# Kernel tuning notes

Hardware: AMD Instinct MI355X
Metric: run time of the kernel (lower is better)

The kernel has to match this reference:

```python
import jax, jax.numpy as jnp
import numpy as np

INPUT_DIM = 1024
NUM_HEADS = 16
D_K = 1024
HEAD_DIM = D_K // NUM_HEADS


def setup_inputs() -> dict:
    key = jax.random.key(0)
    ks = jax.random.split(key, 9)
    s_in = 1.0 / np.sqrt(INPUT_DIM)
    s_dk = 1.0 / np.sqrt(D_K)
    return {
        "x": jax.random.normal(ks[0], (2, 2048, INPUT_DIM), dtype=jnp.float32),
        "Wq": jax.random.uniform(ks[1], (INPUT_DIM, D_K), minval=-s_in, maxval=s_in, dtype=jnp.float32),
        "bq": jax.random.uniform(ks[2], (D_K,), minval=-s_in, maxval=s_in, dtype=jnp.float32),
        "Wk": jax.random.uniform(ks[3], (INPUT_DIM, D_K), minval=-s_in, maxval=s_in, dtype=jnp.float32),
        "bk": jax.random.uniform(ks[4], (D_K,), minval=-s_in, maxval=s_in, dtype=jnp.float32),
        "Wv": jax.random.uniform(ks[5], (INPUT_DIM, D_K), minval=-s_in, maxval=s_in, dtype=jnp.float32),
        "bv": jax.random.uniform(ks[6], (D_K,), minval=-s_in, maxval=s_in, dtype=jnp.float32),
        "Wo": jax.random.uniform(ks[7], (D_K, INPUT_DIM), minval=-s_dk, maxval=s_dk, dtype=jnp.float32),
        "bo": jax.random.uniform(ks[8], (INPUT_DIM,), minval=-s_dk, maxval=s_dk, dtype=jnp.float32),
    }


def reference(x, Wq, bq, Wk, bk, Wv, bv, Wo, bo):
    B, S, _ = x.shape
    H, D = NUM_HEADS, HEAD_DIM
    # QKV projections -> [B, H, S, D]
    q = (x @ Wq + bq).reshape(B, S, H, D).transpose(0, 2, 1, 3)
    k = (x @ Wk + bk).reshape(B, S, H, D).transpose(0, 2, 1, 3)
    v = (x @ Wv + bv).reshape(B, S, H, D).transpose(0, 2, 1, 3)
    scores = jnp.einsum("bhsd,bhtd->bhst", q, k) / jnp.sqrt(jnp.asarray(D, x.dtype))
    attn = jax.nn.softmax(scores, axis=-1)
    out = jnp.einsum("bhst,bhtd->bhsd", attn, v)  # [B,H,S,D]
    out = out.transpose(0, 2, 1, 3).reshape(B, S, H * D)
    return out @ Wo + bo
```

## Files before the change

kernel.cpp:

```cpp
#include <hip/hip_runtime.h>
#include <stdint.h>

typedef _Float16 f16;
typedef f16 f16x4 __attribute__((ext_vector_type(4)));
typedef f16 f16x8 __attribute__((ext_vector_type(8)));
typedef float f32x4 __attribute__((ext_vector_type(4)));
typedef float f32x16 __attribute__((ext_vector_type(16)));

#define AS1 __attribute__((address_space(1)))
#define AS3 __attribute__((address_space(3)))

__device__ __forceinline__ void gll16(const void* g, void* l) {
  __builtin_amdgcn_global_load_lds((AS1 void*)g, (AS3 void*)l, 16, 0, 0);
}

__device__ __forceinline__ f32x4 mfma16(f16x8 a, f16x8 b, f32x4 c) {
  return __builtin_amdgcn_mfma_f32_16x16x32_f16(a, b, c, 0, 0, 0);
}
__device__ __forceinline__ f32x16 mfma32(f16x8 a, f16x8 b, f32x16 c) {
  return __builtin_amdgcn_mfma_f32_32x32x16_f16(a, b, c, 0, 0, 0);
}

__device__ __forceinline__ uint32_t pk_rtn(float a, float b) {
  union { f16 h[2]; uint32_t u; } c;
  c.h[0] = (f16)a;
  c.h[1] = (f16)b;
  return c.u;
}

__device__ __forceinline__ void pl32(uint32_t& x, uint32_t& y) {
  asm("v_permlane32_swap_b32 %0, %1" : "+v"(x), "+v"(y));
}

__device__ __forceinline__ f16x8 mk_bfrag(float e0, float e1, float e2, float e3,
                                          float e4, float e5, float e6, float e7) {
  uint32_t x0 = pk_rtn(e0, e1), y0 = pk_rtn(e4, e5);
  uint32_t x1 = pk_rtn(e2, e3), y1 = pk_rtn(e6, e7);
  pl32(x0, y0);
  pl32(x1, y1);
  union { uint32_t w[4]; f16x8 v; } u;
  u.w[0] = x0; u.w[1] = x1; u.w[2] = y0; u.w[3] = y1;
  return u.v;
}

__device__ __forceinline__ f32x16 zero16() {
  f32x16 z;
#pragma unroll
  for (int i = 0; i < 16; i++) z[i] = 0.f;
  return z;
}


__global__ __launch_bounds__(256) void pack_x_k(const float* __restrict__ x,
                                                f16* __restrict__ xh, int n) {
  int i = (blockIdx.x * 256 + threadIdx.x) * 8;
  if (i < n) {
    float4 a = *(const float4*)(x + i);
    float4 b = *(const float4*)(x + i + 4);
    f16x8 o;
    o[0] = (f16)a.x; o[1] = (f16)a.y; o[2] = (f16)a.z; o[3] = (f16)a.w;
    o[4] = (f16)b.x; o[5] = (f16)b.y; o[6] = (f16)b.z; o[7] = (f16)b.w;
    *(f16x8*)(xh + i) = o;
  }
}

__global__ __launch_bounds__(256) void pack_w_k(const float* __restrict__ Wq,
                                                const float* __restrict__ Wk,
                                                const float* __restrict__ Wv,
                                                const float* __restrict__ Wo,
                                                f16* __restrict__ Wt) {
  __shared__ f16 t[64][65];
  const float* W = (blockIdx.z == 0) ? Wq : (blockIdx.z == 1) ? Wk
                   : (blockIdx.z == 2) ? Wv : Wo;
  int n0 = blockIdx.x * 64, k0 = blockIdx.y * 64;
  int tid = threadIdx.x;
  int kr = tid >> 4;
  int nc = (tid & 15) * 4;
#pragma unroll
  for (int i = 0; i < 4; i++) {
    int k = k0 + kr + i * 16;
    float4 w = *(const float4*)(W + (size_t)k * 1024 + n0 + nc);
    t[nc + 0][kr + i * 16] = (f16)w.x;
    t[nc + 1][kr + i * 16] = (f16)w.y;
    t[nc + 2][kr + i * 16] = (f16)w.z;
    t[nc + 3][kr + i * 16] = (f16)w.w;
  }
  __syncthreads();
  int nr = tid >> 2;
  int c0 = (tid & 3) * 16;
  alignas(16) f16 tmp[16];
#pragma unroll
  for (int e = 0; e < 16; e++) tmp[e] = t[nr][c0 + e];
  f16* dst = Wt + (size_t)(blockIdx.z * 1024 + n0 + nr) * 1024 + k0 + c0;
  *(f16x8*)(dst) = *(const f16x8*)(tmp);
  *(f16x8*)(dst + 8) = *(const f16x8*)(tmp + 8);
}

__device__ __forceinline__ void gemm_main(const f16* __restrict__ A,
                                          const f16* __restrict__ B,
                                          int m0, int n0,
                                          f16* Al, f16* Bl,
                                          f32x4 acc[4][4]) {
  const int K = 1024;
  int tid = threadIdx.x;
  int lane = tid & 63, wid = tid >> 6;
  int wr = (wid >> 1) * 64, wc = (wid & 1) * 64;
#pragma unroll
  for (int mi = 0; mi < 4; mi++)
#pragma unroll
    for (int nj = 0; nj < 4; nj++) {
      f32x4 z = {0.f, 0.f, 0.f, 0.f};
      acc[mi][nj] = z;
    }
  int srow = lane >> 3;
  int sgr = (lane & 7) ^ srow;
  int lr = lane & 15, lg = lane >> 4;
  for (int kt = 0; kt < 16; ++kt) {
    __syncthreads();
#pragma unroll
    for (int q = 0; q < 4; q++) {
      int chunk = wid * 4 + q;
      int row = chunk * 8 + srow;
      gll16(A + (size_t)(m0 + row) * K + kt * 64 + sgr * 8, Al + chunk * 512);
      gll16(B + (size_t)(n0 + row) * K + kt * 64 + sgr * 8, Bl + chunk * 512);
    }
    __syncthreads();
#pragma unroll
    for (int kk = 0; kk < 2; kk++) {
      f16x8 af[4], bf[4];
#pragma unroll
      for (int mi = 0; mi < 4; mi++) {
        int row = wr + mi * 16 + lr;
        int gr = (kk * 4 + lg) ^ (row & 7);
        af[mi] = *(const f16x8*)(Al + row * 64 + gr * 8);
      }
#pragma unroll
      for (int nj = 0; nj < 4; nj++) {
        int row = wc + nj * 16 + lr;
        int gr = (kk * 4 + lg) ^ (row & 7);
        bf[nj] = *(const f16x8*)(Bl + row * 64 + gr * 8);
      }
#pragma unroll
      for (int mi = 0; mi < 4; mi++)
#pragma unroll
        for (int nj = 0; nj < 4; nj++)
          acc[mi][nj] = mfma16(af[mi], bf[nj], acc[mi][nj]);
    }
  }
}

__global__ __launch_bounds__(256) void gemm_qkv_k(const f16* __restrict__ Xh,
                                                  const f16* __restrict__ Wt,
                                                  const float* __restrict__ bq,
                                                  const float* __restrict__ bk,
                                                  const float* __restrict__ bv,
                                                  f16* __restrict__ Q,
                                                  f16* __restrict__ Kb,
                                                  f16* __restrict__ Vt) {
  __shared__ f16 Al[128 * 64];
  __shared__ f16 Bl[128 * 64];
  f32x4 acc[4][4];
  int m0 = blockIdx.y * 128, n0 = blockIdx.x * 128;
  gemm_main(Xh, Wt, m0, n0, Al, Bl, acc);

  int lane = threadIdx.x & 63, wid = threadIdx.x >> 6;
  int wr = (wid >> 1) * 64, wc = (wid & 1) * 64;
  int lg = lane >> 4, lc = lane & 15;
  int which = n0 >> 10;
  if (which == 2) {
#pragma unroll
    for (int mi = 0; mi < 4; mi++)
#pragma unroll
      for (int nj = 0; nj < 4; nj++) {
        int nh = (n0 + wc + nj * 16 + lc) & 1023;
        int h = nh >> 6, d = nh & 63;
        float bb = bv[nh];
        int mbase = m0 + wr + mi * 16 + lg * 4;
        int b = mbase >> 11, s = mbase & 2047;
        f16x4 vv;
#pragma unroll
        for (int r = 0; r < 4; r++) vv[r] = (f16)(acc[mi][nj][r] + bb);
        *(f16x4*)(Vt + ((size_t)(b * 16 + h) * 64 + d) * 2048 + s) = vv;
      }
  } else {
    const float* bias = (which == 0) ? bq : bk;
    f16* out = (which == 0) ? Q : Kb;
    float scale = (which == 0) ? 0.1803368801111204f : 1.0f;
#pragma unroll
    for (int mi = 0; mi < 4; mi++)
#pragma unroll
      for (int nj = 0; nj < 4; nj++) {
        int nh = (n0 + wc + nj * 16 + lc) & 1023;
        int h = nh >> 6, d = nh & 63;
        float bb = bias[nh];
#pragma unroll
        for (int r = 0; r < 4; r++) {
          int m = m0 + wr + mi * 16 + lg * 4 + r;
          int b = m >> 11, s = m & 2047;
          float v = (acc[mi][nj][r] + bb) * scale;
          out[((size_t)(b * 16 + h) * 2048 + s) * 64 + d] = (f16)v;
        }
      }
  }
}

__global__ __launch_bounds__(256) void gemm_out_k(const f16* __restrict__ Oh,
                                                  const f16* __restrict__ Wt,
                                                  const float* __restrict__ bo,
                                                  float* __restrict__ out) {
  __shared__ f16 Al[128 * 64];
  __shared__ f16 Bl[128 * 64];
  f32x4 acc[4][4];
  int m0 = blockIdx.y * 128, n0 = blockIdx.x * 128;
  gemm_main(Oh, Wt, m0, n0, Al, Bl, acc);

  int lane = threadIdx.x & 63, wid = threadIdx.x >> 6;
  int wr = (wid >> 1) * 64, wc = (wid & 1) * 64;
  int lg = lane >> 4, lc = lane & 15;
#pragma unroll
  for (int mi = 0; mi < 4; mi++)
#pragma unroll
    for (int nj = 0; nj < 4; nj++) {
      int n = n0 + wc + nj * 16 + lc;
      float bb = bo[n];
#pragma unroll
      for (int r = 0; r < 4; r++) {
        int m = m0 + wr + mi * 16 + lg * 4 + r;
        out[(size_t)m * 1024 + n] = acc[mi][nj][r] + bb;
      }
    }
}

__global__ __launch_bounds__(128) void attn_k(const f16* __restrict__ Q,
                                              const f16* __restrict__ K,
                                              const f16* __restrict__ Vt,
                                              f16* __restrict__ Oh) {
  __shared__ alignas(16) f16 Kl[2][64 * 64];
  __shared__ alignas(16) f16 Vl[2][64 * 64];

  int tid = threadIdx.x, lane = tid & 63, wid = tid >> 6;
  int q5 = lane & 31, hi = lane >> 5;
  int b0 = blockIdx.x;
  int qc = (b0 >> 3) & 31;
  int bh = (b0 & 7) + ((b0 >> 8) << 3);
  int q0w = qc * 64 + wid * 32;

  const f16* Qp = Q + (size_t)bh * 2048 * 64;
  const f16* Kp = K + (size_t)bh * 2048 * 64;
  const f16* Vp = Vt + (size_t)bh * 64 * 2048;

  f16x8 qf0, qf1, qf2, qf3;
  {
    const f16* qr = Qp + (size_t)(q0w + q5) * 64 + hi * 8;
    qf0 = *(const f16x8*)(qr);
    qf1 = *(const f16x8*)(qr + 16);
    qf2 = *(const f16x8*)(qr + 32);
    qf3 = *(const f16x8*)(qr + 48);
  }

  f32x16 o0 = zero16(), o1 = zero16();
  float m = -1e30f, lsum = 0.f;

  int srow = lane >> 3;
  int sg8 = ((lane & 7) ^ srow) * 8;

  auto STAGE = [&](int buf, int t0) {
#pragma unroll
    for (int qi = 0; qi < 4; qi++) {
      int chunk = wid * 4 + qi;
      int row = chunk * 8 + srow;
      gll16(Kp + (size_t)(t0 + row) * 64 + sg8, &Kl[buf][chunk * 512]);
      gll16(Vp + (size_t)row * 2048 + t0 + sg8, &Vl[buf][chunk * 512]);
    }
  };

  STAGE(0, 0);

  int r0 = q5, r1 = 32 + q5;
  int sw = q5 & 7;

  for (int t = 0; t < 32; ++t) {
    int cur = t & 1;
    if (t < 31) {
      STAGE(cur ^ 1, (t + 1) * 64);
      asm volatile("s_waitcnt vmcnt(8)" ::: "memory");
    } else {
      asm volatile("s_waitcnt vmcnt(0)" ::: "memory");
    }
    __builtin_amdgcn_s_barrier();

    const f16* kb = Kl[cur];
    const f16* vb = Vl[cur];

    f32x16 s0 = zero16(), s1 = zero16();
    __builtin_amdgcn_s_setprio(1);
#pragma unroll
    for (int ks = 0; ks < 4; ks++) {
      int g = 2 * ks + hi;
      f16x8 k0 = *(const f16x8*)(kb + r0 * 64 + ((g ^ sw) << 3));
      f16x8 k1 = *(const f16x8*)(kb + r1 * 64 + ((g ^ sw) << 3));
      f16x8 qv = (ks == 0) ? qf0 : (ks == 1) ? qf1 : (ks == 2) ? qf2 : qf3;
      s0 = mfma32(k0, qv, s0);
      s1 = mfma32(k1, qv, s1);
    }
    __builtin_amdgcn_s_setprio(0);

    f16x8 vf0[4], vf1[4];
#pragma unroll
    for (int ks = 0; ks < 4; ks++) {
      int g = 2 * ks + hi;
      vf0[ks] = *(const f16x8*)(vb + r0 * 64 + ((g ^ sw) << 3));
      vf1[ks] = *(const f16x8*)(vb + r1 * 64 + ((g ^ sw) << 3));
    }

    float w[16];
#pragma unroll
    for (int i = 0; i < 16; i++) w[i] = fmaxf(s0[i], s1[i]);
#pragma unroll
    for (int st = 8; st > 0; st >>= 1)
#pragma unroll
      for (int i = 0; i < st; i++) w[i] = fmaxf(w[i], w[i + st]);
    float mx = w[0];
    mx = fmaxf(mx, __shfl_xor(mx, 32));

    if (__any(mx > m)) {
      float mn = fmaxf(m, mx);
      float al = __builtin_amdgcn_exp2f(m - mn);
      m = mn;
      lsum *= al;
#pragma unroll
      for (int i = 0; i < 16; i++) { o0[i] *= al; o1[i] *= al; }
    }
    float su0 = 0.f, su1 = 0.f, su2 = 0.f, su3 = 0.f;
#pragma unroll
    for (int i = 0; i < 16; i += 4) {
      s0[i + 0] = __builtin_amdgcn_exp2f(s0[i + 0] - m); su0 += s0[i + 0];
      s0[i + 1] = __builtin_amdgcn_exp2f(s0[i + 1] - m); su1 += s0[i + 1];
      s0[i + 2] = __builtin_amdgcn_exp2f(s0[i + 2] - m); su2 += s0[i + 2];
      s0[i + 3] = __builtin_amdgcn_exp2f(s0[i + 3] - m); su3 += s0[i + 3];
    }
#pragma unroll
    for (int i = 0; i < 16; i += 4) {
      s1[i + 0] = __builtin_amdgcn_exp2f(s1[i + 0] - m); su0 += s1[i + 0];
      s1[i + 1] = __builtin_amdgcn_exp2f(s1[i + 1] - m); su1 += s1[i + 1];
      s1[i + 2] = __builtin_amdgcn_exp2f(s1[i + 2] - m); su2 += s1[i + 2];
      s1[i + 3] = __builtin_amdgcn_exp2f(s1[i + 3] - m); su3 += s1[i + 3];
    }
    float sum = (su0 + su1) + (su2 + su3);
    sum += __shfl_xor(sum, 32);
    lsum += sum;

    f16x8 pb0 = mk_bfrag(s0[0], s0[1], s0[2], s0[3], s0[4], s0[5], s0[6], s0[7]);
    f16x8 pb1 = mk_bfrag(s0[8], s0[9], s0[10], s0[11], s0[12], s0[13], s0[14], s0[15]);
    f16x8 pb2 = mk_bfrag(s1[0], s1[1], s1[2], s1[3], s1[4], s1[5], s1[6], s1[7]);
    f16x8 pb3 = mk_bfrag(s1[8], s1[9], s1[10], s1[11], s1[12], s1[13], s1[14], s1[15]);

    __builtin_amdgcn_s_setprio(1);
#pragma unroll
    for (int ks = 0; ks < 4; ks++) {
      f16x8 pv = (ks == 0) ? pb0 : (ks == 1) ? pb1 : (ks == 2) ? pb2 : pb3;
      o0 = mfma32(vf0[ks], pv, o0);
      o1 = mfma32(vf1[ks], pv, o1);
    }
    __builtin_amdgcn_s_setprio(0);

    asm volatile("" ::: "memory");
    __builtin_amdgcn_s_barrier();
  }

  float inv = 1.f / lsum;
  int b = bh >> 4, h = bh & 15;
  f16* op = Oh + ((size_t)(b * 2048 + q0w + q5)) * 1024 + h * 64;
#pragma unroll
  for (int qd = 0; qd < 4; qd++) {
    f16x4 w0, w1;
#pragma unroll
    for (int j = 0; j < 4; j++) {
      int r = qd * 4 + j;
      w0[j] = (f16)(o0[r] * inv);
      w1[j] = (f16)(o1[r] * inv);
    }
    int d0 = 8 * qd + 4 * hi;
    *(f16x4*)(op + d0) = w0;
    *(f16x4*)(op + 32 + d0) = w1;
  }
}


extern "C" void kernel_launch(void* const* d_in, const int* in_sizes, int n_in,
                              void* d_out, int out_size, void* d_ws, size_t ws_size,
                              hipStream_t stream) {
  const float* x  = (const float*)d_in[0];
  const float* Wq = (const float*)d_in[1];
  const float* bq = (const float*)d_in[2];
  const float* Wk = (const float*)d_in[3];
  const float* bk = (const float*)d_in[4];
  const float* Wv = (const float*)d_in[5];
  const float* bv = (const float*)d_in[6];
  const float* Wo = (const float*)d_in[7];
  const float* bo = (const float*)d_in[8];
  float* out = (float*)d_out;

  char* ws = (char*)d_ws;
  const size_t MB8 = (size_t)8 << 20;
  f16* Xh = (f16*)(ws + 0 * MB8);
  f16* Wt = (f16*)(ws + 1 * MB8);
  f16* Q  = (f16*)(ws + 2 * MB8);
  f16* Kb = (f16*)(ws + 3 * MB8);
  f16* Vt = (f16*)(ws + 4 * MB8);
  f16* Oh = (f16*)(ws + 5 * MB8);

  pack_x_k<<<dim3(2048), dim3(256), 0, stream>>>(x, Xh, 4096 * 1024);
  pack_w_k<<<dim3(16, 16, 4), dim3(256), 0, stream>>>(Wq, Wk, Wv, Wo, Wt);
  gemm_qkv_k<<<dim3(24, 32), dim3(256), 0, stream>>>(Xh, Wt, bq, bk, bv, Q, Kb, Vt);
  attn_k<<<dim3(1024), dim3(128), 0, stream>>>(Q, Kb, Vt, Oh);
  gemm_out_k<<<dim3(8, 32), dim3(256), 0, stream>>>(Oh, Wt + (size_t)3072 * 1024, bo, out);
}
```

Baseline: 149.6 us.

## Software-pipeline attention loop so PV MFMAs of previous tile overlap current softmax

Restructures the flash-attention inner loop into a prologue, steady state and epilogue. The P·V product for tile t-1 runs in iteration t, interleaved with the exp2 softmax work of tile t, and the O rescale is deferred by one step. V fragments for the previous tile are read into registers before the buffer is restaged. The aim is to hide the exponential math behind matrix work. The cost is more live registers (vp arrays, P fragments), an extra barrier per iteration and a full vmcnt(0) wait that reduces prefetch depth.

After: 147.7 us. No clear change (-1.3%).

```diff
diff --git a/kernel.cpp b/kernel.cpp
--- a/kernel.cpp
+++ b/kernel.cpp
@@ -279,19 +279,17 @@
   int r0 = q5, r1 = 32 + q5;
   int sw = q5 & 7;
 
-  for (int t = 0; t < 32; ++t) {
-    int cur = t & 1;
-    if (t < 31) {
-      STAGE(cur ^ 1, (t + 1) * 64);
-      asm volatile("s_waitcnt vmcnt(8)" ::: "memory");
-    } else {
-      asm volatile("s_waitcnt vmcnt(0)" ::: "memory");
-    }
+  f16x8 vp0[4], vp1[4];
+  f16x8 pbp0, pbp1, pbp2, pbp3;
+  float aprev = 1.f;
+  bool grew_prev = false;
+
+  {
+    asm volatile("s_waitcnt vmcnt(0)" ::: "memory");
     __builtin_amdgcn_s_barrier();
-
-    const f16* kb = Kl[cur];
-    const f16* vb = Vl[cur];
-
+    STAGE(1, 64);
+
+    const f16* kb = Kl[0];
     f32x16 s0 = zero16(), s1 = zero16();
     __builtin_amdgcn_s_setprio(1);
 #pragma unroll
@@ -305,14 +303,6 @@
     }
     __builtin_amdgcn_s_setprio(0);
 
-    f16x8 vf0[4], vf1[4];
-#pragma unroll
-    for (int ks = 0; ks < 4; ks++) {
-      int g = 2 * ks + hi;
-      vf0[ks] = *(const f16x8*)(vb + r0 * 64 + ((g ^ sw) << 3));
-      vf1[ks] = *(const f16x8*)(vb + r1 * 64 + ((g ^ sw) << 3));
-    }
-
     float w[16];
 #pragma unroll
     for (int i = 0; i < 16; i++) w[i] = fmaxf(s0[i], s1[i]);
@@ -322,50 +312,136 @@
       for (int i = 0; i < st; i++) w[i] = fmaxf(w[i], w[i + st]);
     float mx = w[0];
     mx = fmaxf(mx, __shfl_xor(mx, 32));
-
-    if (__any(mx > m)) {
+    m = mx;
+
+    float sA = 0.f, sB = 0.f, sC = 0.f, sD = 0.f;
+#pragma unroll
+    for (int i = 0; i < 8; i++) { s0[i] = __builtin_amdgcn_exp2f(s0[i] - m); sA += s0[i]; }
+#pragma unroll
+    for (int i = 8; i < 16; i++) { s0[i] = __builtin_amdgcn_exp2f(s0[i] - m); sB += s0[i]; }
+#pragma unroll
+    for (int i = 0; i < 8; i++) { s1[i] = __builtin_amdgcn_exp2f(s1[i] - m); sC += s1[i]; }
+#pragma unroll
+    for (int i = 8; i < 16; i++) { s1[i] = __builtin_amdgcn_exp2f(s1[i] - m); sD += s1[i]; }
+    float sum = (sA + sB) + (sC + sD);
+    sum += __shfl_xor(sum, 32);
+    lsum = sum;
+
+    pbp0 = mk_bfrag(s0[0], s0[1], s0[2], s0[3], s0[4], s0[5], s0[6], s0[7]);
+    pbp1 = mk_bfrag(s0[8], s0[9], s0[10], s0[11], s0[12], s0[13], s0[14], s0[15]);
+    pbp2 = mk_bfrag(s1[0], s1[1], s1[2], s1[3], s1[4], s1[5], s1[6], s1[7]);
+    pbp3 = mk_bfrag(s1[8], s1[9], s1[10], s1[11], s1[12], s1[13], s1[14], s1[15]);
+    aprev = 1.f;
+    grew_prev = false;
+  }
+
+  for (int t = 1; t < 32; ++t) {
+    int cur = t & 1;
+    asm volatile("s_waitcnt vmcnt(0)" ::: "memory");
+    __builtin_amdgcn_s_barrier();
+
+    {
+      const f16* vb = Vl[cur ^ 1];
+#pragma unroll
+      for (int ks = 0; ks < 4; ks++) {
+        int g = 2 * ks + hi;
+        vp0[ks] = *(const f16x8*)(vb + r0 * 64 + ((g ^ sw) << 3));
+        vp1[ks] = *(const f16x8*)(vb + r1 * 64 + ((g ^ sw) << 3));
+      }
+    }
+    asm volatile("s_waitcnt lgkmcnt(0)" ::: "memory");
+    __builtin_amdgcn_sched_barrier(0);
+    __builtin_amdgcn_s_barrier();
+    if (t < 31) STAGE(cur ^ 1, (t + 1) * 64);
+
+    const f16* kb = Kl[cur];
+    f32x16 s0 = zero16(), s1 = zero16();
+    __builtin_amdgcn_s_setprio(1);
+#pragma unroll
+    for (int ks = 0; ks < 4; ks++) {
+      int g = 2 * ks + hi;
+      f16x8 k0 = *(const f16x8*)(kb + r0 * 64 + ((g ^ sw) << 3));
+      f16x8 k1 = *(const f16x8*)(kb + r1 * 64 + ((g ^ sw) << 3));
+      f16x8 qv = (ks == 0) ? qf0 : (ks == 1) ? qf1 : (ks == 2) ? qf2 : qf3;
+      s0 = mfma32(k0, qv, s0);
+      s1 = mfma32(k1, qv, s1);
+    }
+    __builtin_amdgcn_s_setprio(0);
+
+    if (grew_prev) {
+#pragma unroll
+      for (int i = 0; i < 16; i++) { o0[i] *= aprev; o1[i] *= aprev; }
+    }
+
+    float w[16];
+#pragma unroll
+    for (int i = 0; i < 16; i++) w[i] = fmaxf(s0[i], s1[i]);
+#pragma unroll
+    for (int st = 8; st > 0; st >>= 1)
+#pragma unroll
+      for (int i = 0; i < st; i++) w[i] = fmaxf(w[i], w[i + st]);
+    float mx = w[0];
+    mx = fmaxf(mx, __shfl_xor(mx, 32));
+    bool grew = __any(mx > m);
+    float al = 1.f;
+    if (grew) {
       float mn = fmaxf(m, mx);
-      float al = __builtin_amdgcn_exp2f(m - mn);
+      al = __builtin_amdgcn_exp2f(m - mn);
       m = mn;
-      lsum *= al;
-#pragma unroll
-      for (int i = 0; i < 16; i++) { o0[i] *= al; o1[i] *= al; }
-    }
-    float su0 = 0.f, su1 = 0.f, su2 = 0.f, su3 = 0.f;
-#pragma unroll
-    for (int i = 0; i < 16; i += 4) {
-      s0[i + 0] = __builtin_amdgcn_exp2f(s0[i + 0] - m); su0 += s0[i + 0];
-      s0[i + 1] = __builtin_amdgcn_exp2f(s0[i + 1] - m); su1 += s0[i + 1];
-      s0[i + 2] = __builtin_amdgcn_exp2f(s0[i + 2] - m); su2 += s0[i + 2];
-      s0[i + 3] = __builtin_amdgcn_exp2f(s0[i + 3] - m); su3 += s0[i + 3];
-    }
-#pragma unroll
-    for (int i = 0; i < 16; i += 4) {
-      s1[i + 0] = __builtin_amdgcn_exp2f(s1[i + 0] - m); su0 += s1[i + 0];
-      s1[i + 1] = __builtin_amdgcn_exp2f(s1[i + 1] - m); su1 += s1[i + 1];
-      s1[i + 2] = __builtin_amdgcn_exp2f(s1[i + 2] - m); su2 += s1[i + 2];
-      s1[i + 3] = __builtin_amdgcn_exp2f(s1[i + 3] - m); su3 += s1[i + 3];
-    }
-    float sum = (su0 + su1) + (su2 + su3);
+    }
+
+    float sA = 0.f, sB = 0.f, sC = 0.f, sD = 0.f;
+    __builtin_amdgcn_s_setprio(1);
+    o0 = mfma32(vp0[0], pbp0, o0);
+    o1 = mfma32(vp1[0], pbp0, o1);
+#pragma unroll
+    for (int i = 0; i < 8; i++) { s0[i] = __builtin_amdgcn_exp2f(s0[i] - m); sA += s0[i]; }
+    o0 = mfma32(vp0[1], pbp1, o0);
+    o1 = mfma32(vp1[1], pbp1, o1);
+#pragma unroll
+    for (int i = 8; i < 16; i++) { s0[i] = __builtin_amdgcn_exp2f(s0[i] - m); sB += s0[i]; }
+    o0 = mfma32(vp0[2], pbp2, o0);
+    o1 = mfma32(vp1[2], pbp2, o1);
+#pragma unroll
+    for (int i = 0; i < 8; i++) { s1[i] = __builtin_amdgcn_exp2f(s1[i] - m); sC += s1[i]; }
+    o0 = mfma32(vp0[3], pbp3, o0);
+    o1 = mfma32(vp1[3], pbp3, o1);
+#pragma unroll
+    for (int i = 8; i < 16; i++) { s1[i] = __builtin_amdgcn_exp2f(s1[i] - m); sD += s1[i]; }
+    __builtin_amdgcn_s_setprio(0);
+
+    float sum = (sA + sB) + (sC + sD);
     sum += __shfl_xor(sum, 32);
-    lsum += sum;
-
-    f16x8 pb0 = mk_bfrag(s0[0], s0[1], s0[2], s0[3], s0[4], s0[5], s0[6], s0[7]);
-    f16x8 pb1 = mk_bfrag(s0[8], s0[9], s0[10], s0[11], s0[12], s0[13], s0[14], s0[15]);
-    f16x8 pb2 = mk_bfrag(s1[0], s1[1], s1[2], s1[3], s1[4], s1[5], s1[6], s1[7]);
-    f16x8 pb3 = mk_bfrag(s1[8], s1[9], s1[10], s1[11], s1[12], s1[13], s1[14], s1[15]);
-
+    lsum = lsum * al + sum;
+
+    pbp0 = mk_bfrag(s0[0], s0[1], s0[2], s0[3], s0[4], s0[5], s0[6], s0[7]);
+    pbp1 = mk_bfrag(s0[8], s0[9], s0[10], s0[11], s0[12], s0[13], s0[14], s0[15]);
+    pbp2 = mk_bfrag(s1[0], s1[1], s1[2], s1[3], s1[4], s1[5], s1[6], s1[7]);
+    pbp3 = mk_bfrag(s1[8], s1[9], s1[10], s1[11], s1[12], s1[13], s1[14], s1[15]);
+    aprev = al;
+    grew_prev = grew;
+  }
+
+  {
+    const f16* vb = Vl[1];
+#pragma unroll
+    for (int ks = 0; ks < 4; ks++) {
+      int g = 2 * ks + hi;
+      vp0[ks] = *(const f16x8*)(vb + r0 * 64 + ((g ^ sw) << 3));
+      vp1[ks] = *(const f16x8*)(vb + r1 * 64 + ((g ^ sw) << 3));
+    }
+    if (grew_prev) {
+#pragma unroll
+      for (int i = 0; i < 16; i++) { o0[i] *= aprev; o1[i] *= aprev; }
+    }
     __builtin_amdgcn_s_setprio(1);
 #pragma unroll
     for (int ks = 0; ks < 4; ks++) {
-      f16x8 pv = (ks == 0) ? pb0 : (ks == 1) ? pb1 : (ks == 2) ? pb2 : pb3;
-      o0 = mfma32(vf0[ks], pv, o0);
-      o1 = mfma32(vf1[ks], pv, o1);
+      f16x8 pv = (ks == 0) ? pbp0 : (ks == 1) ? pbp1 : (ks == 2) ? pbp2 : pbp3;
+      o0 = mfma32(vp0[ks], pv, o0);
+      o1 = mfma32(vp1[ks], pv, o1);
     }
     __builtin_amdgcn_s_setprio(0);
-
-    asm volatile("" ::: "memory");
-    __builtin_amdgcn_s_barrier();
   }
 
   float inv = 1.f / lsum;
```

## Split attention KV tiles across two waves per query chunk and merge partial softmax

Applied to the files above, without the earlier changes.

The attention kernel now launches 256 threads per block. Two waves cover each 32-query chunk, and each of the pair handles half of every 64-key tile: 32 keys, one score MFMA chain and half the PV work. At the end the two partial (m, l, O) states are combined through LDS with a log-sum-exp style merge before writing fp16 output. Staging is redistributed so two waves load K and two load V, with a 4-way swizzle for the 32-wide V tile. The aim is more waves in flight and shorter per-wave critical paths, at the cost of an extra LDS reduction, doubled per-wave softmax bookkeeping and more barriers.

Result: faster. 144.0 us (-3.7%).

```diff
diff --git a/kernel.cpp b/kernel.cpp
--- a/kernel.cpp
+++ b/kernel.cpp
@@ -231,93 +231,102 @@
     }
 }
 
-__global__ __launch_bounds__(128) void attn_k(const f16* __restrict__ Q,
-                                              const f16* __restrict__ K,
-                                              const f16* __restrict__ Vt,
-                                              f16* __restrict__ Oh) {
-  __shared__ alignas(16) f16 Kl[2][64 * 64];
-  __shared__ alignas(16) f16 Vl[2][64 * 64];
+__global__ __launch_bounds__(256, 4) void attn_k(const f16* __restrict__ Q,
+                                                 const f16* __restrict__ K,
+                                                 const f16* __restrict__ Vt,
+                                                 f16* __restrict__ Oh) {
+  __shared__ alignas(16) char lds_raw[32768];
+  f16* Kl = (f16*)lds_raw;
+  f16* Vl = (f16*)(lds_raw + 16384);
 
   int tid = threadIdx.x, lane = tid & 63, wid = tid >> 6;
   int q5 = lane & 31, hi = lane >> 5;
+  int qc2 = wid >> 1, hv = wid & 1;
   int b0 = blockIdx.x;
   int qc = (b0 >> 3) & 31;
   int bh = (b0 & 7) + ((b0 >> 8) << 3);
-  int q0w = qc * 64 + wid * 32;
+  int q0w = qc * 64 + qc2 * 32;
 
   const f16* Qp = Q + (size_t)bh * 2048 * 64;
   const f16* Kp = K + (size_t)bh * 2048 * 64;
   const f16* Vp = Vt + (size_t)bh * 64 * 2048;
 
-  f16x8 qf0, qf1, qf2, qf3;
+  f16x8 qf[4];
   {
     const f16* qr = Qp + (size_t)(q0w + q5) * 64 + hi * 8;
-    qf0 = *(const f16x8*)(qr);
-    qf1 = *(const f16x8*)(qr + 16);
-    qf2 = *(const f16x8*)(qr + 32);
-    qf3 = *(const f16x8*)(qr + 48);
+#pragma unroll
+    for (int ks = 0; ks < 4; ks++) qf[ks] = *(const f16x8*)(qr + ks * 16);
   }
 
   f32x16 o0 = zero16(), o1 = zero16();
   float m = -1e30f, lsum = 0.f;
 
-  int srow = lane >> 3;
-  int sg8 = ((lane & 7) ^ srow) * 8;
-
-  auto STAGE = [&](int buf, int t0) {
-#pragma unroll
-    for (int qi = 0; qi < 4; qi++) {
-      int chunk = wid * 4 + qi;
-      int row = chunk * 8 + srow;
-      gll16(Kp + (size_t)(t0 + row) * 64 + sg8, &Kl[buf][chunk * 512]);
-      gll16(Vp + (size_t)row * 2048 + t0 + sg8, &Vl[buf][chunk * 512]);
+  int role = wid;
+  int srole = role & 1;
+  int srow8 = lane >> 3, swz8 = ((lane & 7) ^ srow8) * 8;
+  int srow4 = lane >> 2, swz4 = ((lane & 3) ^ (srow4 & 3)) * 8;
+  const f16* sK = Kp + (size_t)(srole * 1024 + srow8) * 64 + swz8;
+  const f16* sV = Vp + (size_t)srow4 * 2048 + srole * 1024 + swz4;
+
+  auto STAGE = [&](int buf, int t) {
+    if (role < 2) {
+      const f16* s = sK + (size_t)t * 32 * 64;
+      f16* d = Kl + buf * 4096 + srole * 2048;
+#pragma unroll
+      for (int c = 0; c < 4; c++) gll16(s + c * 512, d + c * 512);
+    } else {
+      const f16* s = sV + t * 32;
+      f16* d = Vl + buf * 4096 + srole * 2048;
+#pragma unroll
+      for (int c = 0; c < 4; c++) gll16(s + (size_t)c * 16 * 2048, d + c * 512);
     }
   };
 
+  int kqoff[4];
+#pragma unroll
+  for (int ks = 0; ks < 4; ks++) kqoff[ks] = q5 * 64 + (((2 * ks + hi) ^ (q5 & 7)) << 3);
+  int r0 = q5, r1 = q5 + 32;
+  int voff0[2], voff1[2];
+#pragma unroll
+  for (int ks = 0; ks < 2; ks++) {
+    voff0[ks] = r0 * 32 + (((2 * ks + hi) ^ (r0 & 3)) << 3);
+    voff1[ks] = r1 * 32 + (((2 * ks + hi) ^ (r1 & 3)) << 3);
+  }
+
   STAGE(0, 0);
-
-  int r0 = q5, r1 = 32 + q5;
-  int sw = q5 & 7;
 
   for (int t = 0; t < 32; ++t) {
     int cur = t & 1;
     if (t < 31) {
-      STAGE(cur ^ 1, (t + 1) * 64);
-      asm volatile("s_waitcnt vmcnt(8)" ::: "memory");
+      STAGE(cur ^ 1, t + 1);
+      asm volatile("s_waitcnt vmcnt(4)" ::: "memory");
     } else {
       asm volatile("s_waitcnt vmcnt(0)" ::: "memory");
     }
     __builtin_amdgcn_s_barrier();
 
-    const f16* kb = Kl[cur];
-    const f16* vb = Vl[cur];
-
-    f32x16 s0 = zero16(), s1 = zero16();
+    const f16* kb = Kl + cur * 4096 + hv * 2048;
+    const f16* vb = Vl + cur * 4096 + hv * 2048;
+
+    f32x16 s = zero16();
     __builtin_amdgcn_s_setprio(1);
 #pragma unroll
-    for (int ks = 0; ks < 4; ks++) {
-      int g = 2 * ks + hi;
-      f16x8 k0 = *(const f16x8*)(kb + r0 * 64 + ((g ^ sw) << 3));
-      f16x8 k1 = *(const f16x8*)(kb + r1 * 64 + ((g ^ sw) << 3));
-      f16x8 qv = (ks == 0) ? qf0 : (ks == 1) ? qf1 : (ks == 2) ? qf2 : qf3;
-      s0 = mfma32(k0, qv, s0);
-      s1 = mfma32(k1, qv, s1);
-    }
+    for (int ks = 0; ks < 4; ks++)
+      s = mfma32(*(const f16x8*)(kb + kqoff[ks]), qf[ks], s);
     __builtin_amdgcn_s_setprio(0);
 
-    f16x8 vf0[4], vf1[4];
-#pragma unroll
-    for (int ks = 0; ks < 4; ks++) {
-      int g = 2 * ks + hi;
-      vf0[ks] = *(const f16x8*)(vb + r0 * 64 + ((g ^ sw) << 3));
-      vf1[ks] = *(const f16x8*)(vb + r1 * 64 + ((g ^ sw) << 3));
-    }
-
-    float w[16];
-#pragma unroll
-    for (int i = 0; i < 16; i++) w[i] = fmaxf(s0[i], s1[i]);
-#pragma unroll
-    for (int st = 8; st > 0; st >>= 1)
+    f16x8 vf0[2], vf1[2];
+#pragma unroll
+    for (int ks = 0; ks < 2; ks++) {
+      vf0[ks] = *(const f16x8*)(vb + voff0[ks]);
+      vf1[ks] = *(const f16x8*)(vb + voff1[ks]);
+    }
+
+    float w[8];
+#pragma unroll
+    for (int i = 0; i < 8; i++) w[i] = fmaxf(s[i], s[i + 8]);
+#pragma unroll
+    for (int st = 4; st > 0; st >>= 1)
 #pragma unroll
       for (int i = 0; i < st; i++) w[i] = fmaxf(w[i], w[i + st]);
     float mx = w[0];
@@ -331,58 +340,70 @@
 #pragma unroll
       for (int i = 0; i < 16; i++) { o0[i] *= al; o1[i] *= al; }
     }
-    float su0 = 0.f, su1 = 0.f, su2 = 0.f, su3 = 0.f;
-#pragma unroll
-    for (int i = 0; i < 16; i += 4) {
-      s0[i + 0] = __builtin_amdgcn_exp2f(s0[i + 0] - m); su0 += s0[i + 0];
-      s0[i + 1] = __builtin_amdgcn_exp2f(s0[i + 1] - m); su1 += s0[i + 1];
-      s0[i + 2] = __builtin_amdgcn_exp2f(s0[i + 2] - m); su2 += s0[i + 2];
-      s0[i + 3] = __builtin_amdgcn_exp2f(s0[i + 3] - m); su3 += s0[i + 3];
-    }
-#pragma unroll
-    for (int i = 0; i < 16; i += 4) {
-      s1[i + 0] = __builtin_amdgcn_exp2f(s1[i + 0] - m); su0 += s1[i + 0];
-      s1[i + 1] = __builtin_amdgcn_exp2f(s1[i + 1] - m); su1 += s1[i + 1];
-      s1[i + 2] = __builtin_amdgcn_exp2f(s1[i + 2] - m); su2 += s1[i + 2];
-      s1[i + 3] = __builtin_amdgcn_exp2f(s1[i + 3] - m); su3 += s1[i + 3];
-    }
-    float sum = (su0 + su1) + (su2 + su3);
+    float sA = 0.f, sB = 0.f, sC = 0.f, sD = 0.f;
+#pragma unroll
+    for (int i = 0; i < 4; i++)  { s[i] = __builtin_amdgcn_exp2f(s[i] - m);  sA += s[i]; }
+#pragma unroll
+    for (int i = 4; i < 8; i++)  { s[i] = __builtin_amdgcn_exp2f(s[i] - m);  sB += s[i]; }
+#pragma unroll
+    for (int i = 8; i < 12; i++) { s[i] = __builtin_amdgcn_exp2f(s[i] - m);  sC += s[i]; }
+#pragma unroll
+    for (int i = 12; i < 16; i++){ s[i] = __builtin_amdgcn_exp2f(s[i] - m);  sD += s[i]; }
+    float sum = (sA + sB) + (sC + sD);
     sum += __shfl_xor(sum, 32);
     lsum += sum;
 
-    f16x8 pb0 = mk_bfrag(s0[0], s0[1], s0[2], s0[3], s0[4], s0[5], s0[6], s0[7]);
-    f16x8 pb1 = mk_bfrag(s0[8], s0[9], s0[10], s0[11], s0[12], s0[13], s0[14], s0[15]);
-    f16x8 pb2 = mk_bfrag(s1[0], s1[1], s1[2], s1[3], s1[4], s1[5], s1[6], s1[7]);
-    f16x8 pb3 = mk_bfrag(s1[8], s1[9], s1[10], s1[11], s1[12], s1[13], s1[14], s1[15]);
+    f16x8 pb0 = mk_bfrag(s[0], s[1], s[2], s[3], s[4], s[5], s[6], s[7]);
+    f16x8 pb1 = mk_bfrag(s[8], s[9], s[10], s[11], s[12], s[13], s[14], s[15]);
 
     __builtin_amdgcn_s_setprio(1);
-#pragma unroll
-    for (int ks = 0; ks < 4; ks++) {
-      f16x8 pv = (ks == 0) ? pb0 : (ks == 1) ? pb1 : (ks == 2) ? pb2 : pb3;
-      o0 = mfma32(vf0[ks], pv, o0);
-      o1 = mfma32(vf1[ks], pv, o1);
-    }
+    o0 = mfma32(vf0[0], pb0, o0);
+    o0 = mfma32(vf0[1], pb1, o0);
+    o1 = mfma32(vf1[0], pb0, o1);
+    o1 = mfma32(vf1[1], pb1, o1);
     __builtin_amdgcn_s_setprio(0);
 
     asm volatile("" ::: "memory");
     __builtin_amdgcn_s_barrier();
   }
 
-  float inv = 1.f / lsum;
-  int b = bh >> 4, h = bh & 15;
-  f16* op = Oh + ((size_t)(b * 2048 + q0w + q5)) * 1024 + h * 64;
-#pragma unroll
-  for (int qd = 0; qd < 4; qd++) {
-    f16x4 w0, w1;
-#pragma unroll
-    for (int j = 0; j < 4; j++) {
-      int r = qd * 4 + j;
-      w0[j] = (f16)(o0[r] * inv);
-      w1[j] = (f16)(o1[r] * inv);
-    }
-    int d0 = 8 * qd + 4 * hi;
-    *(f16x4*)(op + d0) = w0;
-    *(f16x4*)(op + 32 + d0) = w1;
+  __syncthreads();
+  float* Ox = (float*)lds_raw + qc2 * (32 * 68);
+  float* ml = (float*)lds_raw + 2 * (32 * 68) + qc2 * 64;
+  if (hv == 1) {
+#pragma unroll
+    for (int g = 0; g < 4; g++) {
+      f32x4 a, b;
+#pragma unroll
+      for (int j = 0; j < 4; j++) { a[j] = o0[4 * g + j]; b[j] = o1[4 * g + j]; }
+      *(f32x4*)(Ox + q5 * 68 + 8 * g + 4 * hi) = a;
+      *(f32x4*)(Ox + q5 * 68 + 32 + 8 * g + 4 * hi) = b;
+    }
+    if (hi == 0) { ml[q5 * 2] = m; ml[q5 * 2 + 1] = lsum; }
+  }
+  __syncthreads();
+  if (hv == 0) {
+    float m1 = ml[q5 * 2], l1 = ml[q5 * 2 + 1];
+    float M = fmaxf(m, m1);
+    float w0 = __builtin_amdgcn_exp2f(m - M);
+    float w1 = __builtin_amdgcn_exp2f(m1 - M);
+    float inv = 1.f / (lsum * w0 + l1 * w1);
+    int bB = bh >> 4, hh = bh & 15;
+    f16* op = Oh + ((size_t)(bB * 2048 + q0w + q5)) * 1024 + hh * 64;
+#pragma unroll
+    for (int g = 0; g < 4; g++) {
+      f32x4 x0 = *(const f32x4*)(Ox + q5 * 68 + 8 * g + 4 * hi);
+      f32x4 x1 = *(const f32x4*)(Ox + q5 * 68 + 32 + 8 * g + 4 * hi);
+      f16x4 y0, y1;
+#pragma unroll
+      for (int j = 0; j < 4; j++) {
+        y0[j] = (f16)((o0[4 * g + j] * w0 + x0[j] * w1) * inv);
+        y1[j] = (f16)((o1[4 * g + j] * w0 + x1[j] * w1) * inv);
+      }
+      int d0 = 8 * g + 4 * hi;
+      *(f16x4*)(op + d0) = y0;
+      *(f16x4*)(op + 32 + d0) = y1;
+    }
   }
 }
 
@@ -413,6 +434,6 @@
   pack_x_k<<<dim3(2048), dim3(256), 0, stream>>>(x, Xh, 4096 * 1024);
   pack_w_k<<<dim3(16, 16, 4), dim3(256), 0, stream>>>(Wq, Wk, Wv, Wo, Wt);
   gemm_qkv_k<<<dim3(24, 32), dim3(256), 0, stream>>>(Xh, Wt, bq, bk, bv, Q, Kb, Vt);
-  attn_k<<<dim3(1024), dim3(128), 0, stream>>>(Q, Kb, Vt, Oh);
+  attn_k<<<dim3(1024), dim3(256), 0, stream>>>(Q, Kb, Vt, Oh);
   gemm_out_k<<<dim3(8, 32), dim3(256), 0, stream>>>(Oh, Wt + (size_t)3072 * 1024, bo, out);
 }
```
